# Kernel optimization log

Measured on AMD Instinct MI355X. Metric: run time of the kernel, lower is better.

The kernel has to match this reference:

```python
import math
import jax, jax.numpy as jnp
import numpy as np

_TEMP_CLAMP = 4.6

def _l2n(x):
    # torch F.normalize: x / max(||x||, eps)
    return x / jnp.maximum(jnp.linalg.norm(x, axis=-1, keepdims=True), 1e-12)

def setup_inputs() -> dict:
    key = jax.random.key(0)
    k1, k2, k3, k4, k5 = jax.random.split(key, 5)
    B, S, D, V, NNEG = 1024, 64, 128, 100000, 2048
    hidden = jax.random.normal(k1, (B, S, D), dtype=jnp.float32)
    y = jax.random.randint(k2, (B, S), 0, V, dtype=jnp.int64)
    embed_table = jax.random.normal(k3, (V, D), dtype=jnp.float32)
    sampling_probs = jax.random.uniform(k4, (V,), dtype=jnp.float32, minval=1e-6, maxval=1.0)
    sampled_indices = jax.random.randint(k5, (NNEG,), 0, V, dtype=jnp.int64)
    log_temperature = jnp.asarray(math.log(1.0 / 0.07), dtype=jnp.float32)
    return {"hidden": hidden, "y": y, "embed_table": embed_table,
            "sampling_probs": sampling_probs, "sampled_indices": sampled_indices,
            "log_temperature": log_temperature}

def reference(hidden, y, embed_table, sampling_probs, sampled_indices, log_temperature):
    D = hidden.shape[-1]
    h = hidden.reshape(-1, D)          # [N, D]
    yf = y.reshape(-1)                 # [N]
    valid = (yf != 0)                  # padding mask (static-shape weighting instead of boolean gather)

    true_p = sampling_probs[yf]                # [N]
    samp_p = sampling_probs[sampled_indices]   # [NNEG]
    e_pos = embed_table[yf]                    # [N, D]
    e_neg = embed_table[sampled_indices]       # [NNEG, D]

    temp = jnp.exp(jnp.minimum(log_temperature, _TEMP_CLAMP))
    hn = _l2n(h)
    pos_logits = jnp.sum(hn * _l2n(e_pos), axis=-1) * temp        # [N]
    neg_logits = (hn @ _l2n(e_neg).T) * temp                      # [N, NNEG]

    collision = yf[:, None] == sampled_indices[None, :]
    neg_logits = jnp.where(collision, -1e9, neg_logits)

    pos_adj = pos_logits - jnp.log(true_p + 1e-10)                # [N]
    neg_adj = neg_logits - jnp.log(samp_p + 1e-10)[None, :]       # [N, NNEG]
    logits = jnp.concatenate([pos_adj[:, None], neg_adj], axis=1) # [N, 1+NNEG]

    per_row = -jax.nn.log_softmax(logits, axis=-1)[:, 0]          # CE with label 0
    w = valid.astype(per_row.dtype)
    return jnp.sum(per_row * w) / jnp.maximum(jnp.sum(w), 1.0)
```

## Files before the change

kernel.cpp:

```cpp
#include <hip/hip_runtime.h>
#include <math.h>

#define TPB 256
#define NNEG 2048
#define D 128
#define L2E 1.44269504088896340736f

typedef __attribute__((ext_vector_type(8))) short bf16x8;
typedef __attribute__((ext_vector_type(4))) float f32x4;

#define MFMA16 __builtin_amdgcn_mfma_f32_16x16x32_bf16

static __device__ __forceinline__ unsigned int f2bf(float f) {
    unsigned int u = __float_as_uint(f);
    return (u + 0x7FFFu + ((u >> 16) & 1u)) >> 16;
}

__global__ __launch_bounds__(TPB) void sspe_prep(
    const float* __restrict__ embed,
    const float* __restrict__ sprobs,
    const int* __restrict__ sidx,
    unsigned int* __restrict__ en_bf,
    float* __restrict__ ln_samp)
{
    const int t = threadIdx.x;
    const int wave = t >> 6;
    const int lane = t & 63;
    const int j = blockIdx.x * 4 + wave;
    const int idx = sidx[j];

    float2 v = reinterpret_cast<const float2*>(embed)[(size_t)idx * 64 + lane];
    float ss = v.x * v.x + v.y * v.y;
    ss += __shfl_xor(ss, 1);
    ss += __shfl_xor(ss, 2);
    ss += __shfl_xor(ss, 4);
    ss += __shfl_xor(ss, 8);
    ss += __shfl_xor(ss, 16);
    ss += __shfl_xor(ss, 32);
    const float rinv = 1.0f / fmaxf(sqrtf(ss), 1e-12f);
    en_bf[(size_t)j * 64 + lane] = f2bf(v.x * rinv) | (f2bf(v.y * rinv) << 16);
    if (lane == 0) ln_samp[j] = logf(sprobs[idx] + 1e-10f);
}

static __device__ __forceinline__ void compute_tile(
    const bf16x8 (&A)[4][4], const bf16x8 (&B)[4], const float lk, const int ci,
    const int (&yv)[4][4], float (&l)[4][4], const float t2, const float M2)
{
    f32x4 c[4];
    #pragma unroll
    for (int rt = 0; rt < 4; ++rt) c[rt] = (f32x4){0.f, 0.f, 0.f, 0.f};
    #pragma unroll
    for (int ks = 0; ks < 4; ++ks)
        #pragma unroll
        for (int rt = 0; rt < 4; ++rt)
            c[rt] = MFMA16(A[rt][ks], B[ks], c[rt], 0, 0, 0);
    const float nl2 = fmaf(lk, -L2E, -M2);
    #pragma unroll
    for (int rt = 0; rt < 4; ++rt)
        #pragma unroll
        for (int j = 0; j < 4; ++j) {
            const float a = fmaf(c[rt][j], t2, nl2);
            const float e = __builtin_amdgcn_exp2f(a);
            l[rt][j] += (ci == yv[rt][j]) ? 0.0f : e;
        }
}

#define LOADB(B, LK, CI, it) do {                                  \
    const unsigned char* q_ = pB + (size_t)(it) * 4096;            \
    B[0] = *reinterpret_cast<const bf16x8*>(q_);                   \
    B[1] = *reinterpret_cast<const bf16x8*>(q_ + 64);              \
    B[2] = *reinterpret_cast<const bf16x8*>(q_ + 128);             \
    B[3] = *reinterpret_cast<const bf16x8*>(q_ + 192);             \
    LK = pL[(it) * 16];                                            \
    CI = pI[(it) * 16];                                            \
} while (0)

__global__ __launch_bounds__(TPB, 2) void sspe_main(
    const float* __restrict__ hidden,
    const int* __restrict__ y,
    const float* __restrict__ embed,
    const float* __restrict__ sprobs,
    const int* __restrict__ sidx,
    const float* __restrict__ ltemp,
    const unsigned int* __restrict__ en_bf,
    const float* __restrict__ ln_samp,
    float2* __restrict__ partials)
{
    const int t = threadIdx.x;
    const int wave = t >> 6;
    const int lane = t & 63;
    const int rb = blockIdx.x * 64;

    __shared__ __align__(16) unsigned char hs[64 * 256];
    __shared__ float pos_s[64];
    __shared__ int   ys[64];
    __shared__ float sred[4][64];

    const float temp = __builtin_amdgcn_exp2f(fminf(ltemp[0], 4.6f) * L2E);
    const float t2 = temp * L2E;
    const float Mln = temp + 14.0f;
    const float M2 = Mln * L2E;

    if (t < 64) ys[t] = y[rb + t];
    __syncthreads();

    #pragma unroll 1
    for (int i = 0; i < 16; i += 4) {
        float2 h2[4], e2[4];
        int yi[4];
        #pragma unroll
        for (int u = 0; u < 4; ++u) {
            const int lr = wave * 16 + i + u;
            h2[u] = reinterpret_cast<const float2*>(hidden)[(size_t)(rb + lr) * 64 + lane];
            yi[u] = ys[lr];
        }
        #pragma unroll
        for (int u = 0; u < 4; ++u)
            e2[u] = reinterpret_cast<const float2*>(embed)[(size_t)yi[u] * 64 + lane];
        float ss[4], es[4], dt[4];
        #pragma unroll
        for (int u = 0; u < 4; ++u) {
            ss[u] = h2[u].x * h2[u].x + h2[u].y * h2[u].y;
            es[u] = e2[u].x * e2[u].x + e2[u].y * e2[u].y;
            dt[u] = h2[u].x * e2[u].x + h2[u].y * e2[u].y;
        }
        #pragma unroll
        for (int m = 1; m <= 32; m <<= 1)
            #pragma unroll
            for (int u = 0; u < 4; ++u) {
                ss[u] += __shfl_xor(ss[u], m);
                es[u] += __shfl_xor(es[u], m);
                dt[u] += __shfl_xor(dt[u], m);
            }
        #pragma unroll
        for (int u = 0; u < 4; ++u) {
            const int lr = wave * 16 + i + u;
            const float rinv = 1.0f / fmaxf(sqrtf(ss[u]), 1e-12f);
            const unsigned int uu = f2bf(h2[u].x * rinv) | (f2bf(h2[u].y * rinv) << 16);
            const int rx = (lr & 7) << 4;
            *reinterpret_cast<unsigned int*>(hs + lr * 256 + ((lane * 4) ^ rx)) = uu;
            if (lane == 0)
                pos_s[lr] = dt[u] * rinv * (1.0f / fmaxf(sqrtf(es[u]), 1e-12f)) * temp
                            - logf(sprobs[yi[u]] + 1e-10f);
        }
    }
    __syncthreads();

    bf16x8 A[4][4];
    #pragma unroll
    for (int rt = 0; rt < 4; ++rt) {
        const int row = rt * 16 + (lane & 15);
        const int rx = (row & 7) << 4;
        const unsigned char* rp = hs + row * 256;
        #pragma unroll
        for (int ks = 0; ks < 4; ++ks) {
            const int col = ((ks * 64) + ((lane >> 4) << 4)) ^ rx;
            A[rt][ks] = *reinterpret_cast<const bf16x8*>(rp + col);
        }
    }

    int yv[4][4];
    float l[4][4];
    #pragma unroll
    for (int rt = 0; rt < 4; ++rt)
        #pragma unroll
        for (int j = 0; j < 4; ++j) {
            yv[rt][j] = ys[rt * 16 + ((lane >> 4) << 2) + j];
            l[rt][j] = 0.0f;
        }

    const int nw = wave * 512;
    const unsigned char* pB = reinterpret_cast<const unsigned char*>(en_bf)
                            + (size_t)(nw + (lane & 15)) * 256 + ((lane >> 4) << 4);
    const float* pL = ln_samp + nw + (lane & 15);
    const int* pI = sidx + nw + (lane & 15);

    bf16x8 B0[4], B1[4];
    float lk0, lk1;
    int ci0, ci1;

    LOADB(B0, lk0, ci0, 0);
    #pragma unroll 1
    for (int nb = 0; nb < 30; nb += 2) {
        LOADB(B1, lk1, ci1, nb + 1);
        compute_tile(A, B0, lk0, ci0, yv, l, t2, M2);
        LOADB(B0, lk0, ci0, nb + 2);
        compute_tile(A, B1, lk1, ci1, yv, l, t2, M2);
    }
    LOADB(B1, lk1, ci1, 31);
    compute_tile(A, B0, lk0, ci0, yv, l, t2, M2);
    compute_tile(A, B1, lk1, ci1, yv, l, t2, M2);

    #pragma unroll
    for (int rt = 0; rt < 4; ++rt)
        #pragma unroll
        for (int j = 0; j < 4; ++j) {
            float v = l[rt][j];
            v += __shfl_xor(v, 1);
            v += __shfl_xor(v, 2);
            v += __shfl_xor(v, 4);
            v += __shfl_xor(v, 8);
            l[rt][j] = v;
        }
    if ((lane & 15) == 0) {
        #pragma unroll
        for (int rt = 0; rt < 4; ++rt)
            #pragma unroll
            for (int j = 0; j < 4; ++j)
                sred[wave][rt * 16 + ((lane >> 4) << 2) + j] = l[rt][j];
    }
    __syncthreads();

    if (t < 64) {
        const float s = sred[0][t] + sred[1][t] + sred[2][t] + sred[3][t];
        const float pa = pos_s[t];
        const float stot = s + __builtin_amdgcn_exp2f(fmaf(pa, L2E, -M2));
        float per = Mln + logf(stot) - pa;
        float w = (ys[t] != 0) ? 1.0f : 0.0f;
        per *= w;
        #pragma unroll
        for (int msk = 1; msk < 64; msk <<= 1) {
            per += __shfl_xor(per, msk);
            w += __shfl_xor(w, msk);
        }
        if (t == 0) partials[blockIdx.x] = make_float2(per, w);
    }
}

__global__ __launch_bounds__(TPB) void sspe_finalize(
    const float2* __restrict__ partials, int n, float* __restrict__ out)
{
    __shared__ float ssum[TPB];
    __shared__ float scnt[TPB];
    const int t = threadIdx.x;
    float s = 0.0f, c = 0.0f;
    for (int i = t; i < n; i += TPB) {
        const float2 p = partials[i];
        s += p.x; c += p.y;
    }
    ssum[t] = s; scnt[t] = c;
    __syncthreads();
    for (int k = TPB / 2; k > 0; k >>= 1) {
        if (t < k) { ssum[t] += ssum[t + k]; scnt[t] += scnt[t + k]; }
        __syncthreads();
    }
    if (t == 0) out[0] = ssum[0] / fmaxf(scnt[0], 1.0f);
}

extern "C" void kernel_launch(void* const* d_in, const int* in_sizes, int n_in,
                              void* d_out, int out_size, void* d_ws, size_t ws_size,
                              hipStream_t stream) {
    const float* hidden = (const float*)d_in[0];
    const int*   yv     = (const int*)d_in[1];
    const float* embed  = (const float*)d_in[2];
    const float* sprobs = (const float*)d_in[3];
    const int*   sidx   = (const int*)d_in[4];
    const float* ltemp  = (const float*)d_in[5];
    float* out = (float*)d_out;

    const int nrows = in_sizes[1];
    const int nblocks = nrows / 64;

    char* w = (char*)d_ws;
    unsigned int* en_bf  = (unsigned int*)w;
    float*  ln_samp      = (float*)(w + (size_t)NNEG * D * 2);
    float2* partials     = (float2*)(w + (size_t)NNEG * D * 2 + NNEG * 4);

    sspe_prep<<<NNEG / 4, TPB, 0, stream>>>(embed, sprobs, sidx, en_bf, ln_samp);
    sspe_main<<<nblocks, TPB, 0, stream>>>(hidden, yv, embed, sprobs, sidx, ltemp,
                                           en_bf, ln_samp, partials);
    sspe_finalize<<<1, TPB, 0, stream>>>(partials, nblocks, out);
}
```

Baseline: 98.49 us.

## Stage negative embeddings in LDS via async global_load_lds with row-split waves

Changes the work split so each wave owns 16 hidden rows across all negatives instead of all 64 rows over a quarter of the negatives. Negative embedding chunks are staged into double-buffered swizzled LDS with global_load_lds and shared by all four waves. This removes per-wave direct global B loads and cuts register pressure (A fragments shrink to 4), allowing 4 blocks per CU. The cost is a block-wide barrier per 64-negative chunk and four times as many LDS reads of B per MFMA.

```diff
diff --git a/kernel.cpp b/kernel.cpp
--- a/kernel.cpp
+++ b/kernel.cpp
@@ -4,6 +4,8 @@
 #define TPB 256
 #define NNEG 2048
 #define D 128
+#define CHUNK 64
+#define NCH (NNEG / CHUNK)
 #define L2E 1.44269504088896340736f
 
 typedef __attribute__((ext_vector_type(8))) short bf16x8;
@@ -14,6 +16,12 @@
 static __device__ __forceinline__ unsigned int f2bf(float f) {
     unsigned int u = __float_as_uint(f);
     return (u + 0x7FFFu + ((u >> 16) & 1u)) >> 16;
+}
+
+static __device__ __forceinline__ void stage16(const void* g, void* l) {
+    __builtin_amdgcn_global_load_lds(
+        (const __attribute__((address_space(1))) unsigned int*)g,
+        (__attribute__((address_space(3))) unsigned int*)l, 16, 0, 0);
 }
 
 __global__ __launch_bounds__(TPB) void sspe_prep(
@@ -42,40 +50,7 @@
     if (lane == 0) ln_samp[j] = logf(sprobs[idx] + 1e-10f);
 }
 
-static __device__ __forceinline__ void compute_tile(
-    const bf16x8 (&A)[4][4], const bf16x8 (&B)[4], const float lk, const int ci,
-    const int (&yv)[4][4], float (&l)[4][4], const float t2, const float M2)
-{
-    f32x4 c[4];
-    #pragma unroll
-    for (int rt = 0; rt < 4; ++rt) c[rt] = (f32x4){0.f, 0.f, 0.f, 0.f};
-    #pragma unroll
-    for (int ks = 0; ks < 4; ++ks)
-        #pragma unroll
-        for (int rt = 0; rt < 4; ++rt)
-            c[rt] = MFMA16(A[rt][ks], B[ks], c[rt], 0, 0, 0);
-    const float nl2 = fmaf(lk, -L2E, -M2);
-    #pragma unroll
-    for (int rt = 0; rt < 4; ++rt)
-        #pragma unroll
-        for (int j = 0; j < 4; ++j) {
-            const float a = fmaf(c[rt][j], t2, nl2);
-            const float e = __builtin_amdgcn_exp2f(a);
-            l[rt][j] += (ci == yv[rt][j]) ? 0.0f : e;
-        }
-}
-
-#define LOADB(B, LK, CI, it) do {                                  \
-    const unsigned char* q_ = pB + (size_t)(it) * 4096;            \
-    B[0] = *reinterpret_cast<const bf16x8*>(q_);                   \
-    B[1] = *reinterpret_cast<const bf16x8*>(q_ + 64);              \
-    B[2] = *reinterpret_cast<const bf16x8*>(q_ + 128);             \
-    B[3] = *reinterpret_cast<const bf16x8*>(q_ + 192);             \
-    LK = pL[(it) * 16];                                            \
-    CI = pI[(it) * 16];                                            \
-} while (0)
-
-__global__ __launch_bounds__(TPB, 2) void sspe_main(
+__global__ __launch_bounds__(TPB, 4) void sspe_main(
     const float* __restrict__ hidden,
     const int* __restrict__ y,
     const float* __restrict__ embed,
@@ -91,10 +66,10 @@
     const int lane = t & 63;
     const int rb = blockIdx.x * 64;
 
-    __shared__ __align__(16) unsigned char hs[64 * 256];
+    __shared__ __align__(16) unsigned char smem[2 * CHUNK * 256];
     __shared__ float pos_s[64];
     __shared__ int   ys[64];
-    __shared__ float sred[4][64];
+    __shared__ float sums[64];
 
     const float temp = __builtin_amdgcn_exp2f(fminf(ltemp[0], 4.6f) * L2E);
     const float t2 = temp * L2E;
@@ -138,7 +113,7 @@
             const float rinv = 1.0f / fmaxf(sqrtf(ss[u]), 1e-12f);
             const unsigned int uu = f2bf(h2[u].x * rinv) | (f2bf(h2[u].y * rinv) << 16);
             const int rx = (lr & 7) << 4;
-            *reinterpret_cast<unsigned int*>(hs + lr * 256 + ((lane * 4) ^ rx)) = uu;
+            *reinterpret_cast<unsigned int*>(smem + lr * 256 + ((lane * 4) ^ rx)) = uu;
             if (lane == 0)
                 pos_s[lr] = dt[u] * rinv * (1.0f / fmaxf(sqrtf(es[u]), 1e-12f)) * temp
                             - logf(sprobs[yi[u]] + 1e-10f);
@@ -146,73 +121,105 @@
     }
     __syncthreads();
 
-    bf16x8 A[4][4];
-    #pragma unroll
-    for (int rt = 0; rt < 4; ++rt) {
-        const int row = rt * 16 + (lane & 15);
-        const int rx = (row & 7) << 4;
-        const unsigned char* rp = hs + row * 256;
-        #pragma unroll
-        for (int ks = 0; ks < 4; ++ks) {
-            const int col = ((ks * 64) + ((lane >> 4) << 4)) ^ rx;
-            A[rt][ks] = *reinterpret_cast<const bf16x8*>(rp + col);
-        }
-    }
-
-    int yv[4][4];
-    float l[4][4];
-    #pragma unroll
-    for (int rt = 0; rt < 4; ++rt)
-        #pragma unroll
-        for (int j = 0; j < 4; ++j) {
-            yv[rt][j] = ys[rt * 16 + ((lane >> 4) << 2) + j];
-            l[rt][j] = 0.0f;
-        }
-
-    const int nw = wave * 512;
-    const unsigned char* pB = reinterpret_cast<const unsigned char*>(en_bf)
-                            + (size_t)(nw + (lane & 15)) * 256 + ((lane >> 4) << 4);
-    const float* pL = ln_samp + nw + (lane & 15);
-    const int* pI = sidx + nw + (lane & 15);
-
-    bf16x8 B0[4], B1[4];
-    float lk0, lk1;
-    int ci0, ci1;
-
-    LOADB(B0, lk0, ci0, 0);
+    bf16x8 A[4];
+    {
+        const int row = wave * 16 + (lane & 15);
+        const int rx = (lane & 7) << 4;
+        const unsigned char* rp = smem + row * 256;
+        #pragma unroll
+        for (int ks = 0; ks < 4; ++ks)
+            A[ks] = *reinterpret_cast<const bf16x8*>(
+                rp + ((ks * 64 + ((lane >> 4) << 4)) ^ rx));
+    }
+    __syncthreads();
+
+    const int cj = lane & 15;
+    const int rgrp = lane >> 4;
+    int yv[4];
+    float l[4];
+    #pragma unroll
+    for (int j = 0; j < 4; ++j) {
+        yv[j] = ys[wave * 16 + rgrp * 4 + j];
+        l[j] = 0.0f;
+    }
+
+    unsigned int soff[4];
+    #pragma unroll
+    for (int i = 0; i < 4; ++i) {
+        const unsigned int doff = i * 4096 + wave * 1024 + lane * 16;
+        soff[i] = doff ^ (((doff >> 8) & 7) << 4);
+    }
+    const unsigned char* en = reinterpret_cast<const unsigned char*>(en_bf);
+    const int rx = (cj & 7) << 4;
+
+    #pragma unroll
+    for (int i = 0; i < 4; ++i)
+        stage16(en + soff[i], smem + i * 4096 + wave * 1024);
+
     #pragma unroll 1
-    for (int nb = 0; nb < 30; nb += 2) {
-        LOADB(B1, lk1, ci1, nb + 1);
-        compute_tile(A, B0, lk0, ci0, yv, l, t2, M2);
-        LOADB(B0, lk0, ci0, nb + 2);
-        compute_tile(A, B1, lk1, ci1, yv, l, t2, M2);
-    }
-    LOADB(B1, lk1, ci1, 31);
-    compute_tile(A, B0, lk0, ci0, yv, l, t2, M2);
-    compute_tile(A, B1, lk1, ci1, yv, l, t2, M2);
-
-    #pragma unroll
-    for (int rt = 0; rt < 4; ++rt)
-        #pragma unroll
-        for (int j = 0; j < 4; ++j) {
-            float v = l[rt][j];
-            v += __shfl_xor(v, 1);
-            v += __shfl_xor(v, 2);
-            v += __shfl_xor(v, 4);
-            v += __shfl_xor(v, 8);
-            l[rt][j] = v;
-        }
-    if ((lane & 15) == 0) {
-        #pragma unroll
-        for (int rt = 0; rt < 4; ++rt)
-            #pragma unroll
-            for (int j = 0; j < 4; ++j)
-                sred[wave][rt * 16 + ((lane >> 4) << 2) + j] = l[rt][j];
+    for (int ch = 0; ch < NCH; ++ch) {
+        const int cur = (ch & 1) << 14;
+        const int nxt = cur ^ 16384;
+        __syncthreads();
+
+        float lk[4];
+        int ci[4];
+        #pragma unroll
+        for (int tt = 0; tt < 4; ++tt) {
+            lk[tt] = ln_samp[ch * 64 + tt * 16 + cj];
+            ci[tt] = sidx[ch * 64 + tt * 16 + cj];
+        }
+
+        if (ch + 1 < NCH) {
+            const unsigned char* enn = en + (size_t)(ch + 1) * 16384;
+            #pragma unroll
+            for (int i = 0; i < 4; ++i)
+                stage16(enn + soff[i], smem + nxt + i * 4096 + wave * 1024);
+        }
+
+        f32x4 c[4];
+        #pragma unroll
+        for (int tt = 0; tt < 4; ++tt) {
+            const unsigned char* bp = smem + cur + (tt * 16 + cj) * 256;
+            c[tt] = (f32x4){0.f, 0.f, 0.f, 0.f};
+            #pragma unroll
+            for (int ks = 0; ks < 4; ++ks) {
+                const bf16x8 b = *reinterpret_cast<const bf16x8*>(
+                    bp + ((ks * 64 + (rgrp << 4)) ^ rx));
+                c[tt] = MFMA16(A[ks], b, c[tt], 0, 0, 0);
+            }
+        }
+
+        #pragma unroll
+        for (int tt = 0; tt < 4; ++tt) {
+            const float nl2 = fmaf(lk[tt], -L2E, -M2);
+            #pragma unroll
+            for (int j = 0; j < 4; ++j) {
+                const float a = fmaf(c[tt][j], t2, nl2);
+                const float e = __builtin_amdgcn_exp2f(a);
+                l[j] += (ci[tt] == yv[j]) ? 0.0f : e;
+            }
+        }
+    }
+
+    #pragma unroll
+    for (int j = 0; j < 4; ++j) {
+        float v = l[j];
+        v += __shfl_xor(v, 1);
+        v += __shfl_xor(v, 2);
+        v += __shfl_xor(v, 4);
+        v += __shfl_xor(v, 8);
+        l[j] = v;
+    }
+    if (cj == 0) {
+        #pragma unroll
+        for (int j = 0; j < 4; ++j)
+            sums[wave * 16 + rgrp * 4 + j] = l[j];
     }
     __syncthreads();
 
     if (t < 64) {
-        const float s = sred[0][t] + sred[1][t] + sred[2][t] + sred[3][t];
+        const float s = sums[t];
         const float pa = pos_s[t];
         const float stot = s + __builtin_amdgcn_exp2f(fmaf(pa, L2E, -M2));
         float per = Mln + logf(stot) - pa;
```

New measurement: 80.53 us. -18.2%, faster.
